# Optimization experiments

Hardware: AMD Instinct MI355X
Metric: run time of the kernel (lower is better)

## Reference

```python
import jax, jax.numpy as jnp
from jax import lax
import numpy as np

T, B, C, H = 2048, 512, 8, 20  # seq_len, batch, input channels, hidden size


def _lstm_layer(x_seq, W_ih, W_hh, b_ih, b_hh):
    """One unidirectional LSTM layer, PyTorch gate order (i, f, g, o).
    x_seq: [T, B, in], W_ih: [4H, in], W_hh: [4H, H]. Returns h sequence [T, B, H]."""
    Hh = W_hh.shape[1]
    # Precompute input contribution for all timesteps (batched GEMM, off the scan critical path)
    gx = jnp.einsum('tbc,gc->tbg', x_seq, W_ih) + b_ih + b_hh  # [T, B, 4H]

    def step(carry, g_t):
        h, c = carry
        g = g_t + h @ W_hh.T  # [B, 4H]
        i, f, gg, o = jnp.split(g, 4, axis=-1)
        i = jax.nn.sigmoid(i)
        f = jax.nn.sigmoid(f)
        gg = jnp.tanh(gg)
        o = jax.nn.sigmoid(o)
        c = f * c + i * gg
        h = o * jnp.tanh(c)
        return (h, c), h

    b = x_seq.shape[1]
    h0 = jnp.zeros((b, Hh), x_seq.dtype)
    c0 = jnp.zeros((b, Hh), x_seq.dtype)
    _, ys = lax.scan(step, (h0, c0), gx)
    return ys


def setup_inputs() -> dict:
    key = jax.random.key(0)
    ks = jax.random.split(key, 9)
    s = 1.0 / np.sqrt(H)  # PyTorch LSTM init scale
    return {
        'x': jax.random.normal(ks[0], (T, B, C), jnp.float32),
        'W_ih0': jax.random.uniform(ks[1], (4 * H, C), jnp.float32, -s, s),
        'W_hh0': jax.random.uniform(ks[2], (4 * H, H), jnp.float32, -s, s),
        'b_ih0': jax.random.uniform(ks[3], (4 * H,), jnp.float32, -s, s),
        'b_hh0': jax.random.uniform(ks[4], (4 * H,), jnp.float32, -s, s),
        'W_ih1': jax.random.uniform(ks[5], (4 * H, H), jnp.float32, -s, s),
        'W_hh1': jax.random.uniform(ks[6], (4 * H, H), jnp.float32, -s, s),
        'b_ih1': jax.random.uniform(ks[7], (4 * H,), jnp.float32, -s, s),
        'b_hh1': jax.random.uniform(ks[8], (4 * H,), jnp.float32, -s, s),
    }


def reference(x, W_ih0, W_hh0, b_ih0, b_hh0, W_ih1, W_hh1, b_ih1, b_hh1):
    # 2-layer LSTM with zero initial states; forward returns the full output sequence
    # (the fc head in the original module is unused in forward()).
    h1 = _lstm_layer(x, W_ih0, W_hh0, b_ih0, b_hh0)   # [T, B, H]
    out = _lstm_layer(h1, W_ih1, W_hh1, b_ih1, b_hh1)  # [T, B, H]
    return out
```

## Files before the change

kernel.cpp:

```cpp
#include <hip/hip_runtime.h>

namespace {

typedef float v2f __attribute__((ext_vector_type(2)));

constexpr int T_SEQ = 2048;
constexpr int B_SZ  = 512;
constexpr int C_IN  = 8;
constexpr int H_SZ  = 20;
constexpr int P_LEN = 16;
constexpr int N_PH  = T_SEQ / P_LEN;
constexpr int RING  = 2 * P_LEN;
constexpr float LOG2E = 1.44269504088896340736f;

__device__ __forceinline__ float rlane(float v, int lane) {
  return __int_as_float(__builtin_amdgcn_readlane(__float_as_int(v), lane));
}

template<int S>
__device__ __forceinline__ float quad_bcast(float v) {
  return __int_as_float(__builtin_amdgcn_update_dpp(
      __float_as_int(v), __float_as_int(v), S * 0x55, 0xF, 0xF, true));
}

__device__ __forceinline__ v2f fma2(v2f a, v2f b, v2f c) {
  return __builtin_elementwise_fma(a, b, c);
}
__device__ __forceinline__ v2f splat2(float s) { v2f r; r.x = s; r.y = s; return r; }
__device__ __forceinline__ v2f zero2() { v2f r; r.x = 0.f; r.y = 0.f; return r; }

__device__ __forceinline__ v2f act2(v2f a, float cm, float am, float ad) {
  float ex = __builtin_amdgcn_exp2f(a.x * cm);
  float ey = __builtin_amdgcn_exp2f(a.y * cm);
  float sx = __builtin_amdgcn_rcpf(1.0f + ex);
  float sy = __builtin_amdgcn_rcpf(1.0f + ey);
  v2f r; r.x = __fmaf_rn(sx, am, ad); r.y = __fmaf_rn(sy, am, ad);
  return r;
}

__device__ __forceinline__ float fast_tanh(float a) {
  float e = __builtin_amdgcn_exp2f(a * (-2.0f * LOG2E));
  float s = __builtin_amdgcn_rcpf(1.0f + e);
  return __fmaf_rn(s, 2.0f, -1.0f);
}

#define H_BCAST(ha, hb, k) (((k) < 16) ? rlane((ha), 4 * (k)) : rlane((hb), 4 * ((k) - 16)))

__global__ __attribute__((amdgpu_flat_work_group_size(128, 128),
                          amdgpu_waves_per_eu(1, 1)))
void lstm2_pk(const float* __restrict__ x,
              const float* __restrict__ Wih0, const float* __restrict__ Whh0,
              const float* __restrict__ bih0, const float* __restrict__ bhh0,
              const float* __restrict__ Wih1, const float* __restrict__ Whh1,
              const float* __restrict__ bih1, const float* __restrict__ bhh1,
              float* __restrict__ out)
{
  __shared__ __align__(16) float hbuf[RING][H_SZ];
  __shared__ __align__(16) float xbuf[2][P_LEN * C_IN];

  const int tid = threadIdx.x;
  const int wv  = tid >> 6;
  const int l   = tid & 63;
  const int b   = blockIdx.x;
  const int k1  = l >> 2;
  const int g   = l & 3;
  const int k2  = 16 + (k1 & 3);
  const int j1  = g * H_SZ + k1;
  const int j2  = g * H_SZ + k2;

  const bool  isg = (g == 2);
  const float cm  = isg ? (-2.0f * LOG2E) : (-LOG2E);
  const float am  = isg ?  2.0f : 1.0f;
  const float ad  = isg ? -1.0f : 0.0f;

  if (wv == 0) {
    v2f wx1[C_IN / 2], wx2[C_IN / 2];
    v2f wh[H_SZ];
#pragma unroll
    for (int t = 0; t < C_IN / 2; ++t) {
      wx1[t].x = Wih0[j1 * C_IN + 2 * t]; wx1[t].y = Wih0[j1 * C_IN + 2 * t + 1];
      wx2[t].x = Wih0[j2 * C_IN + 2 * t]; wx2[t].y = Wih0[j2 * C_IN + 2 * t + 1];
    }
#pragma unroll
    for (int k = 0; k < H_SZ; ++k) {
      wh[k].x = Whh0[j1 * H_SZ + k]; wh[k].y = Whh0[j2 * H_SZ + k];
    }
    v2f bias2; bias2.x = bih0[j1] + bhh0[j1]; bias2.y = bih0[j2] + bhh0[j2];

    float ha = 0.f, ca = 0.f, hb = 0.f, cb = 0.f;

    const float* xl = x + (size_t)(l >> 3) * (B_SZ * C_IN) + b * C_IN + (l & 7);
    const size_t halfph = (size_t)8 * B_SZ * C_IN;
    const size_t phstr  = (size_t)P_LEN * B_SZ * C_IN;

    {
      float v0 = xl[0], v1 = xl[halfph];
      xbuf[0][l] = v0; xbuf[0][64 + l] = v1;
    }
    float n0 = xl[phstr], n1 = xl[phstr + halfph];

    for (int p = 0; p <= N_PH; ++p) {
      if (p < N_PH) {
        const int buf = p & 1;
        float4 xc0 = ((const float4*)&xbuf[buf][0])[0];
        float4 xc1 = ((const float4*)&xbuf[buf][0])[1];
        for (int j = 0; j < P_LEN; ++j) {
          const int n = p * P_LEN + j;
          v2f xp[4];
          xp[0].x = xc0.x; xp[0].y = xc0.y; xp[1].x = xc0.z; xp[1].y = xc0.w;
          xp[2].x = xc1.x; xp[2].y = xc1.y; xp[3].x = xc1.z; xp[3].y = xc1.w;
          if (j + 1 < P_LEN) {
            xc0 = ((const float4*)&xbuf[buf][(j + 1) * C_IN])[0];
            xc1 = ((const float4*)&xbuf[buf][(j + 1) * C_IN])[1];
          }

          v2f A0 = bias2, A1 = zero2();
#pragma unroll
          for (int k = 0; k < H_SZ; k += 2) {
            float h0 = H_BCAST(ha, hb, k);
            float h1 = H_BCAST(ha, hb, k + 1);
            A0 = fma2(wh[k],     splat2(h0), A0);
            A1 = fma2(wh[k + 1], splat2(h1), A1);
          }
          v2f X1 = zero2(), X2 = zero2();
#pragma unroll
          for (int t = 0; t < C_IN / 2; ++t) {
            X1 = fma2(wx1[t], xp[t], X1);
            X2 = fma2(wx2[t], xp[t], X2);
          }
          v2f A = A0 + A1;
          A.x += X1.x + X1.y;
          A.y += X2.x + X2.y;

          v2f act = act2(A, cm, am, ad);
          float iv = quad_bcast<0>(act.x), fv = quad_bcast<1>(act.x);
          float gv = quad_bcast<2>(act.x), ov = quad_bcast<3>(act.x);
          ca = __fmaf_rn(fv, ca, iv * gv);
          ha = ov * fast_tanh(ca);
          iv = quad_bcast<0>(act.y); fv = quad_bcast<1>(act.y);
          gv = quad_bcast<2>(act.y); ov = quad_bcast<3>(act.y);
          cb = __fmaf_rn(fv, cb, iv * gv);
          hb = ov * fast_tanh(cb);

          const int slot = n & (RING - 1);
          if (g == 0) {
            hbuf[slot][k1] = ha;
            if (k1 < 4) hbuf[slot][16 + k1] = hb;
          }
        }
        if (p + 1 < N_PH) { xbuf[(p + 1) & 1][l] = n0; xbuf[(p + 1) & 1][64 + l] = n1; }
        if (p + 2 < N_PH) {
          n0 = xl[(size_t)(p + 2) * phstr];
          n1 = xl[(size_t)(p + 2) * phstr + halfph];
        }
      }
      __syncthreads();
    }
  } else {
    v2f wy1[H_SZ / 2], wy2[H_SZ / 2];
    v2f wq[H_SZ];
#pragma unroll
    for (int t = 0; t < H_SZ / 2; ++t) {
      wy1[t].x = Wih1[j1 * H_SZ + 2 * t]; wy1[t].y = Wih1[j1 * H_SZ + 2 * t + 1];
      wy2[t].x = Wih1[j2 * H_SZ + 2 * t]; wy2[t].y = Wih1[j2 * H_SZ + 2 * t + 1];
    }
#pragma unroll
    for (int k = 0; k < H_SZ; ++k) {
      wq[k].x = Whh1[j1 * H_SZ + k]; wq[k].y = Whh1[j2 * H_SZ + k];
    }
    v2f bias2; bias2.x = bih1[j1] + bhh1[j1]; bias2.y = bih1[j2] + bhh1[j2];

    float ha = 0.f, ca = 0.f, hb = 0.f, cb = 0.f;
    float* op = out + b * H_SZ;

    auto stepW1 = [&](int n, const float4 (&yq)[5]) {
      v2f yp[H_SZ / 2];
      yp[0].x = yq[0].x; yp[0].y = yq[0].y; yp[1].x = yq[0].z; yp[1].y = yq[0].w;
      yp[2].x = yq[1].x; yp[2].y = yq[1].y; yp[3].x = yq[1].z; yp[3].y = yq[1].w;
      yp[4].x = yq[2].x; yp[4].y = yq[2].y; yp[5].x = yq[2].z; yp[5].y = yq[2].w;
      yp[6].x = yq[3].x; yp[6].y = yq[3].y; yp[7].x = yq[3].z; yp[7].y = yq[3].w;
      yp[8].x = yq[4].x; yp[8].y = yq[4].y; yp[9].x = yq[4].z; yp[9].y = yq[4].w;

      v2f Y1a = zero2(), Y1b = zero2(), Y2a = zero2(), Y2b = zero2();
#pragma unroll
      for (int t = 0; t < H_SZ / 2; t += 2) {
        Y1a = fma2(wy1[t],     yp[t],     Y1a);
        Y2a = fma2(wy2[t],     yp[t],     Y2a);
        Y1b = fma2(wy1[t + 1], yp[t + 1], Y1b);
        Y2b = fma2(wy2[t + 1], yp[t + 1], Y2b);
      }
      v2f Q0 = bias2, Q1 = zero2();
#pragma unroll
      for (int k = 0; k < H_SZ; k += 2) {
        float q0 = H_BCAST(ha, hb, k);
        float q1 = H_BCAST(ha, hb, k + 1);
        Q0 = fma2(wq[k],     splat2(q0), Q0);
        Q1 = fma2(wq[k + 1], splat2(q1), Q1);
      }
      v2f A = Q0 + Q1;
      v2f Y1 = Y1a + Y1b, Y2 = Y2a + Y2b;
      A.x += Y1.x + Y1.y;
      A.y += Y2.x + Y2.y;

      v2f act = act2(A, cm, am, ad);
      float iv = quad_bcast<0>(act.x), fv = quad_bcast<1>(act.x);
      float gv = quad_bcast<2>(act.x), ov = quad_bcast<3>(act.x);
      ca = __fmaf_rn(fv, ca, iv * gv);
      ha = ov * fast_tanh(ca);
      iv = quad_bcast<0>(act.y); fv = quad_bcast<1>(act.y);
      gv = quad_bcast<2>(act.y); ov = quad_bcast<3>(act.y);
      cb = __fmaf_rn(fv, cb, iv * gv);
      hb = ov * fast_tanh(cb);

      if (g == 0) {
        op[k1] = ha;
        if (k1 < 4) op[16 + k1] = hb;
      }
      op += B_SZ * H_SZ;
    };

    for (int p = 0; p <= N_PH; ++p) {
      if (p >= 1) {
        const int base = (p - 1) * P_LEN;
        float4 yA[5], yB[5];
        {
          const float4* s = (const float4*)hbuf[base & (RING - 1)];
          yA[0] = s[0]; yA[1] = s[1]; yA[2] = s[2]; yA[3] = s[3]; yA[4] = s[4];
        }
        {
          const float4* s = (const float4*)hbuf[(base + 1) & (RING - 1)];
          yB[0] = s[0]; yB[1] = s[1]; yB[2] = s[2]; yB[3] = s[3]; yB[4] = s[4];
        }
        for (int jj = 0; jj < P_LEN; jj += 2) {
          stepW1(base + jj, yA);
          if (jj + 2 < P_LEN) {
            const float4* s = (const float4*)hbuf[(base + jj + 2) & (RING - 1)];
            yA[0] = s[0]; yA[1] = s[1]; yA[2] = s[2]; yA[3] = s[3]; yA[4] = s[4];
          }
          stepW1(base + jj + 1, yB);
          if (jj + 3 < P_LEN) {
            const float4* s = (const float4*)hbuf[(base + jj + 3) & (RING - 1)];
            yB[0] = s[0]; yB[1] = s[1]; yB[2] = s[2]; yB[3] = s[3]; yB[4] = s[4];
          }
        }
      }
      __syncthreads();
    }
  }
}

}

extern "C" void kernel_launch(void* const* d_in, const int* in_sizes, int n_in,
                              void* d_out, int out_size, void* d_ws, size_t ws_size,
                              hipStream_t stream) {
  const float* x    = (const float*)d_in[0];
  const float* Wih0 = (const float*)d_in[1];
  const float* Whh0 = (const float*)d_in[2];
  const float* bih0 = (const float*)d_in[3];
  const float* bhh0 = (const float*)d_in[4];
  const float* Wih1 = (const float*)d_in[5];
  const float* Whh1 = (const float*)d_in[6];
  const float* bih1 = (const float*)d_in[7];
  const float* bhh1 = (const float*)d_in[8];
  float* out = (float*)d_out;

  hipLaunchKernelGGL(lstm2_pk, dim3(B_SZ), dim3(128), 0, stream,
                     x, Wih0, Whh0, bih0, bhh0, Wih1, Whh1, bih1, bhh1, out);
}
```

Before: 704.4 us.

## Offload half of layer-1 input projection to layer-0 wave and rebalance recurrent FMAs

The layer-0 wave now computes the first 10 terms of layer 1's input projection (W_ih1 times h1) right after producing each h1, and passes the partial sums to the layer-1 wave through a new LDS ring buffer. This balances work between the two pipelined waves. Both waves now broadcast h once into a register array right after computing it, so the next step's recurrent dot product uses four independent accumulators instead of readlanes placed inside the FMA chain. The tanh*o product is also folded into a single fma. The layer-0 wave takes on extra FMAs, registers and LDS writes on its critical path.

```diff
diff --git a/kernel.cpp b/kernel.cpp
--- a/kernel.cpp
+++ b/kernel.cpp
@@ -12,6 +12,7 @@
 constexpr int N_PH  = T_SEQ / P_LEN;
 constexpr int RING  = 2 * P_LEN;
 constexpr float LOG2E = 1.44269504088896340736f;
+constexpr float M2 = -2.0f * LOG2E;
 
 __device__ __forceinline__ float rlane(float v, int lane) {
   return __int_as_float(__builtin_amdgcn_readlane(__float_as_int(v), lane));
@@ -37,14 +38,6 @@
   v2f r; r.x = __fmaf_rn(sx, am, ad); r.y = __fmaf_rn(sy, am, ad);
   return r;
 }
-
-__device__ __forceinline__ float fast_tanh(float a) {
-  float e = __builtin_amdgcn_exp2f(a * (-2.0f * LOG2E));
-  float s = __builtin_amdgcn_rcpf(1.0f + e);
-  return __fmaf_rn(s, 2.0f, -1.0f);
-}
-
-#define H_BCAST(ha, hb, k) (((k) < 16) ? rlane((ha), 4 * (k)) : rlane((hb), 4 * ((k) - 16)))
 
 __global__ __attribute__((amdgpu_flat_work_group_size(128, 128),
                           amdgpu_waves_per_eu(1, 1)))
@@ -56,6 +49,7 @@
               float* __restrict__ out)
 {
   __shared__ __align__(16) float hbuf[RING][H_SZ];
+  __shared__ __align__(16) v2f   pbuf[RING][64];
   __shared__ __align__(16) float xbuf[2][P_LEN * C_IN];
 
   const int tid = threadIdx.x;
@@ -76,6 +70,7 @@
   if (wv == 0) {
     v2f wx1[C_IN / 2], wx2[C_IN / 2];
     v2f wh[H_SZ];
+    v2f wp[10];
 #pragma unroll
     for (int t = 0; t < C_IN / 2; ++t) {
       wx1[t].x = Wih0[j1 * C_IN + 2 * t]; wx1[t].y = Wih0[j1 * C_IN + 2 * t + 1];
@@ -85,8 +80,15 @@
     for (int k = 0; k < H_SZ; ++k) {
       wh[k].x = Whh0[j1 * H_SZ + k]; wh[k].y = Whh0[j2 * H_SZ + k];
     }
+#pragma unroll
+    for (int k = 0; k < 10; ++k) {
+      wp[k].x = Wih1[j1 * H_SZ + k]; wp[k].y = Wih1[j2 * H_SZ + k];
+    }
     v2f bias2; bias2.x = bih0[j1] + bhh0[j1]; bias2.y = bih0[j2] + bhh0[j2];
 
+    float h_s[H_SZ];
+#pragma unroll
+    for (int k = 0; k < H_SZ; ++k) h_s[k] = 0.f;
     float ha = 0.f, ca = 0.f, hb = 0.f, cb = 0.f;
 
     const float* xl = x + (size_t)(l >> 3) * (B_SZ * C_IN) + b * C_IN + (l & 7);
@@ -114,39 +116,60 @@
             xc1 = ((const float4*)&xbuf[buf][(j + 1) * C_IN])[1];
           }
 
-          v2f A0 = bias2, A1 = zero2();
-#pragma unroll
-          for (int k = 0; k < H_SZ; k += 2) {
-            float h0 = H_BCAST(ha, hb, k);
-            float h1 = H_BCAST(ha, hb, k + 1);
-            A0 = fma2(wh[k],     splat2(h0), A0);
-            A1 = fma2(wh[k + 1], splat2(h1), A1);
-          }
           v2f X1 = zero2(), X2 = zero2();
 #pragma unroll
           for (int t = 0; t < C_IN / 2; ++t) {
             X1 = fma2(wx1[t], xp[t], X1);
             X2 = fma2(wx2[t], xp[t], X2);
           }
-          v2f A = A0 + A1;
-          A.x += X1.x + X1.y;
-          A.y += X2.x + X2.y;
+          v2f Xs; Xs.x = X1.x + X1.y; Xs.y = X2.x + X2.y;
+
+          v2f A0 = bias2, A1 = Xs, A2 = zero2(), A3 = zero2();
+#pragma unroll
+          for (int k = 0; k < H_SZ; k += 4) {
+            A0 = fma2(wh[k],     splat2(h_s[k]),     A0);
+            A1 = fma2(wh[k + 1], splat2(h_s[k + 1]), A1);
+            A2 = fma2(wh[k + 2], splat2(h_s[k + 2]), A2);
+            A3 = fma2(wh[k + 3], splat2(h_s[k + 3]), A3);
+          }
+          v2f A = (A0 + A1) + (A2 + A3);
 
           v2f act = act2(A, cm, am, ad);
           float iv = quad_bcast<0>(act.x), fv = quad_bcast<1>(act.x);
           float gv = quad_bcast<2>(act.x), ov = quad_bcast<3>(act.x);
           ca = __fmaf_rn(fv, ca, iv * gv);
-          ha = ov * fast_tanh(ca);
+          {
+            float e = __builtin_amdgcn_exp2f(ca * M2);
+            float r = __builtin_amdgcn_rcpf(1.0f + e);
+            ha = __fmaf_rn(r, ov + ov, -ov);
+          }
           iv = quad_bcast<0>(act.y); fv = quad_bcast<1>(act.y);
           gv = quad_bcast<2>(act.y); ov = quad_bcast<3>(act.y);
           cb = __fmaf_rn(fv, cb, iv * gv);
-          hb = ov * fast_tanh(cb);
+          {
+            float e = __builtin_amdgcn_exp2f(cb * M2);
+            float r = __builtin_amdgcn_rcpf(1.0f + e);
+            hb = __fmaf_rn(r, ov + ov, -ov);
+          }
 
           const int slot = n & (RING - 1);
           if (g == 0) {
             hbuf[slot][k1] = ha;
             if (k1 < 4) hbuf[slot][16 + k1] = hb;
           }
+
+#pragma unroll
+          for (int k = 0; k < 16; ++k) h_s[k] = rlane(ha, 4 * k);
+#pragma unroll
+          for (int k = 0; k < 4; ++k)  h_s[16 + k] = rlane(hb, 4 * k);
+
+          v2f P0 = zero2(), P1 = zero2();
+#pragma unroll
+          for (int k = 0; k < 10; k += 2) {
+            P0 = fma2(wp[k],     splat2(h_s[k]),     P0);
+            P1 = fma2(wp[k + 1], splat2(h_s[k + 1]), P1);
+          }
+          pbuf[slot][l] = P0 + P1;
         }
         if (p + 1 < N_PH) { xbuf[(p + 1) & 1][l] = n0; xbuf[(p + 1) & 1][64 + l] = n1; }
         if (p + 2 < N_PH) {
@@ -157,90 +180,111 @@
       __syncthreads();
     }
   } else {
-    v2f wy1[H_SZ / 2], wy2[H_SZ / 2];
+    v2f wy1[5], wy2[5];
+#pragma unroll
+    for (int t = 0; t < 5; ++t) {
+      wy1[t].x = Wih1[j1 * H_SZ + 10 + 2 * t]; wy1[t].y = Wih1[j1 * H_SZ + 11 + 2 * t];
+      wy2[t].x = Wih1[j2 * H_SZ + 10 + 2 * t]; wy2[t].y = Wih1[j2 * H_SZ + 11 + 2 * t];
+    }
     v2f wq[H_SZ];
-#pragma unroll
-    for (int t = 0; t < H_SZ / 2; ++t) {
-      wy1[t].x = Wih1[j1 * H_SZ + 2 * t]; wy1[t].y = Wih1[j1 * H_SZ + 2 * t + 1];
-      wy2[t].x = Wih1[j2 * H_SZ + 2 * t]; wy2[t].y = Wih1[j2 * H_SZ + 2 * t + 1];
-    }
 #pragma unroll
     for (int k = 0; k < H_SZ; ++k) {
       wq[k].x = Whh1[j1 * H_SZ + k]; wq[k].y = Whh1[j2 * H_SZ + k];
     }
     v2f bias2; bias2.x = bih1[j1] + bhh1[j1]; bias2.y = bih1[j2] + bhh1[j2];
 
+    float h_s[H_SZ];
+#pragma unroll
+    for (int k = 0; k < H_SZ; ++k) h_s[k] = 0.f;
     float ha = 0.f, ca = 0.f, hb = 0.f, cb = 0.f;
     float* op = out + b * H_SZ;
 
-    auto stepW1 = [&](int n, const float4 (&yq)[5]) {
-      v2f yp[H_SZ / 2];
-      yp[0].x = yq[0].x; yp[0].y = yq[0].y; yp[1].x = yq[0].z; yp[1].y = yq[0].w;
-      yp[2].x = yq[1].x; yp[2].y = yq[1].y; yp[3].x = yq[1].z; yp[3].y = yq[1].w;
-      yp[4].x = yq[2].x; yp[4].y = yq[2].y; yp[5].x = yq[2].z; yp[5].y = yq[2].w;
-      yp[6].x = yq[3].x; yp[6].y = yq[3].y; yp[7].x = yq[3].z; yp[7].y = yq[3].w;
-      yp[8].x = yq[4].x; yp[8].y = yq[4].y; yp[9].x = yq[4].z; yp[9].y = yq[4].w;
-
+    auto stepW1 = [&](const float4 (&yq)[3], v2f P) {
+      v2f yp[5];
+      yp[0].x = yq[0].z; yp[0].y = yq[0].w;
+      yp[1].x = yq[1].x; yp[1].y = yq[1].y;
+      yp[2].x = yq[1].z; yp[2].y = yq[1].w;
+      yp[3].x = yq[2].x; yp[3].y = yq[2].y;
+      yp[4].x = yq[2].z; yp[4].y = yq[2].w;
       v2f Y1a = zero2(), Y1b = zero2(), Y2a = zero2(), Y2b = zero2();
-#pragma unroll
-      for (int t = 0; t < H_SZ / 2; t += 2) {
-        Y1a = fma2(wy1[t],     yp[t],     Y1a);
-        Y2a = fma2(wy2[t],     yp[t],     Y2a);
-        Y1b = fma2(wy1[t + 1], yp[t + 1], Y1b);
-        Y2b = fma2(wy2[t + 1], yp[t + 1], Y2b);
-      }
-      v2f Q0 = bias2, Q1 = zero2();
-#pragma unroll
-      for (int k = 0; k < H_SZ; k += 2) {
-        float q0 = H_BCAST(ha, hb, k);
-        float q1 = H_BCAST(ha, hb, k + 1);
-        Q0 = fma2(wq[k],     splat2(q0), Q0);
-        Q1 = fma2(wq[k + 1], splat2(q1), Q1);
-      }
-      v2f A = Q0 + Q1;
+      Y1a = fma2(wy1[0], yp[0], Y1a); Y2a = fma2(wy2[0], yp[0], Y2a);
+      Y1b = fma2(wy1[1], yp[1], Y1b); Y2b = fma2(wy2[1], yp[1], Y2b);
+      Y1a = fma2(wy1[2], yp[2], Y1a); Y2a = fma2(wy2[2], yp[2], Y2a);
+      Y1b = fma2(wy1[3], yp[3], Y1b); Y2b = fma2(wy2[3], yp[3], Y2b);
+      Y1a = fma2(wy1[4], yp[4], Y1a); Y2a = fma2(wy2[4], yp[4], Y2a);
       v2f Y1 = Y1a + Y1b, Y2 = Y2a + Y2b;
-      A.x += Y1.x + Y1.y;
-      A.y += Y2.x + Y2.y;
+      v2f Ys; Ys.x = Y1.x + Y1.y; Ys.y = Y2.x + Y2.y;
+
+      v2f Q0 = bias2, Q1 = P, Q2 = Ys, Q3 = zero2();
+#pragma unroll
+      for (int k = 0; k < H_SZ; k += 4) {
+        Q0 = fma2(wq[k],     splat2(h_s[k]),     Q0);
+        Q1 = fma2(wq[k + 1], splat2(h_s[k + 1]), Q1);
+        Q2 = fma2(wq[k + 2], splat2(h_s[k + 2]), Q2);
+        Q3 = fma2(wq[k + 3], splat2(h_s[k + 3]), Q3);
+      }
+      v2f A = (Q0 + Q1) + (Q2 + Q3);
 
       v2f act = act2(A, cm, am, ad);
       float iv = quad_bcast<0>(act.x), fv = quad_bcast<1>(act.x);
       float gv = quad_bcast<2>(act.x), ov = quad_bcast<3>(act.x);
       ca = __fmaf_rn(fv, ca, iv * gv);
-      ha = ov * fast_tanh(ca);
+      {
+        float e = __builtin_amdgcn_exp2f(ca * M2);
+        float r = __builtin_amdgcn_rcpf(1.0f + e);
+        ha = __fmaf_rn(r, ov + ov, -ov);
+      }
       iv = quad_bcast<0>(act.y); fv = quad_bcast<1>(act.y);
       gv = quad_bcast<2>(act.y); ov = quad_bcast<3>(act.y);
       cb = __fmaf_rn(fv, cb, iv * gv);
-      hb = ov * fast_tanh(cb);
+      {
+        float e = __builtin_amdgcn_exp2f(cb * M2);
+        float r = __builtin_amdgcn_rcpf(1.0f + e);
+        hb = __fmaf_rn(r, ov + ov, -ov);
+      }
 
       if (g == 0) {
         op[k1] = ha;
         if (k1 < 4) op[16 + k1] = hb;
       }
       op += B_SZ * H_SZ;
+
+#pragma unroll
+      for (int k = 0; k < 16; ++k) h_s[k] = rlane(ha, 4 * k);
+#pragma unroll
+      for (int k = 0; k < 4; ++k)  h_s[16 + k] = rlane(hb, 4 * k);
     };
 
     for (int p = 0; p <= N_PH; ++p) {
       if (p >= 1) {
         const int base = (p - 1) * P_LEN;
-        float4 yA[5], yB[5];
+        float4 yA[3], yB[3]; v2f pA, pB;
         {
-          const float4* s = (const float4*)hbuf[base & (RING - 1)];
-          yA[0] = s[0]; yA[1] = s[1]; yA[2] = s[2]; yA[3] = s[3]; yA[4] = s[4];
+          const int s0 = base & (RING - 1);
+          const float4* s = (const float4*)hbuf[s0];
+          yA[0] = s[2]; yA[1] = s[3]; yA[2] = s[4];
+          pA = pbuf[s0][l];
         }
         {
-          const float4* s = (const float4*)hbuf[(base + 1) & (RING - 1)];
-          yB[0] = s[0]; yB[1] = s[1]; yB[2] = s[2]; yB[3] = s[3]; yB[4] = s[4];
+          const int s1 = (base + 1) & (RING - 1);
+          const float4* s = (const float4*)hbuf[s1];
+          yB[0] = s[2]; yB[1] = s[3]; yB[2] = s[4];
+          pB = pbuf[s1][l];
         }
         for (int jj = 0; jj < P_LEN; jj += 2) {
-          stepW1(base + jj, yA);
+          stepW1(yA, pA);
           if (jj + 2 < P_LEN) {
-            const float4* s = (const float4*)hbuf[(base + jj + 2) & (RING - 1)];
-            yA[0] = s[0]; yA[1] = s[1]; yA[2] = s[2]; yA[3] = s[3]; yA[4] = s[4];
-          }
-          stepW1(base + jj + 1, yB);
+            const int sn = (base + jj + 2) & (RING - 1);
+            const float4* s = (const float4*)hbuf[sn];
+            yA[0] = s[2]; yA[1] = s[3]; yA[2] = s[4];
+            pA = pbuf[sn][l];
+          }
+          stepW1(yB, pB);
           if (jj + 3 < P_LEN) {
-            const float4* s = (const float4*)hbuf[(base + jj + 3) & (RING - 1)];
-            yB[0] = s[0]; yB[1] = s[1]; yB[2] = s[2]; yB[3] = s[3]; yB[4] = s[4];
+            const int sn = (base + jj + 3) & (RING - 1);
+            const float4* s = (const float4*)hbuf[sn];
+            yB[0] = s[2]; yB[1] = s[3]; yB[2] = s[4];
+            pB = pbuf[sn][l];
           }
         }
       }
```

After: 731.6 us. 1.04x slower.

## Split LSTM into three-wave pipeline with dedicated input-projection wave

Applied to the files above, without the earlier changes.

Adds a third wavefront that computes the input projections (W_ih0·x and W_ih1·h1) for each phase ahead of time and stages them in shared-memory rings. The two recurrent waves then only do the hidden-state matvec and activations on the serial critical path. The aim is to take the input-GEMM work off the recurrence latency chain. The cost is an extra wave per block, more LDS, and a deeper three-stage barrier pipeline that adds two extra phases of sync.

```diff
diff --git a/kernel.cpp b/kernel.cpp
--- a/kernel.cpp
+++ b/kernel.cpp
@@ -46,9 +46,9 @@
 
 #define H_BCAST(ha, hb, k) (((k) < 16) ? rlane((ha), 4 * (k)) : rlane((hb), 4 * ((k) - 16)))
 
-__global__ __attribute__((amdgpu_flat_work_group_size(128, 128),
+__global__ __attribute__((amdgpu_flat_work_group_size(192, 192),
                           amdgpu_waves_per_eu(1, 1)))
-void lstm2_pk(const float* __restrict__ x,
+void lstm2_3w(const float* __restrict__ x,
               const float* __restrict__ Wih0, const float* __restrict__ Whh0,
               const float* __restrict__ bih0, const float* __restrict__ bhh0,
               const float* __restrict__ Wih1, const float* __restrict__ Whh1,
@@ -56,7 +56,9 @@
               float* __restrict__ out)
 {
   __shared__ __align__(16) float hbuf[RING][H_SZ];
-  __shared__ __align__(16) float xbuf[2][P_LEN * C_IN];
+  __shared__ __align__(16) v2f   ybuf[RING][64];
+  __shared__ __align__(16) v2f   xsbuf[RING][64];
+  __shared__ __align__(16) float xbuf[P_LEN * C_IN];
 
   const int tid = threadIdx.x;
   const int wv  = tid >> 6;
@@ -74,13 +76,7 @@
   const float ad  = isg ? -1.0f : 0.0f;
 
   if (wv == 0) {
-    v2f wx1[C_IN / 2], wx2[C_IN / 2];
     v2f wh[H_SZ];
-#pragma unroll
-    for (int t = 0; t < C_IN / 2; ++t) {
-      wx1[t].x = Wih0[j1 * C_IN + 2 * t]; wx1[t].y = Wih0[j1 * C_IN + 2 * t + 1];
-      wx2[t].x = Wih0[j2 * C_IN + 2 * t]; wx2[t].y = Wih0[j2 * C_IN + 2 * t + 1];
-    }
 #pragma unroll
     for (int k = 0; k < H_SZ; ++k) {
       wh[k].x = Whh0[j1 * H_SZ + k]; wh[k].y = Whh0[j2 * H_SZ + k];
@@ -89,32 +85,18 @@
 
     float ha = 0.f, ca = 0.f, hb = 0.f, cb = 0.f;
 
-    const float* xl = x + (size_t)(l >> 3) * (B_SZ * C_IN) + b * C_IN + (l & 7);
-    const size_t halfph = (size_t)8 * B_SZ * C_IN;
-    const size_t phstr  = (size_t)P_LEN * B_SZ * C_IN;
-
-    {
-      float v0 = xl[0], v1 = xl[halfph];
-      xbuf[0][l] = v0; xbuf[0][64 + l] = v1;
-    }
-    float n0 = xl[phstr], n1 = xl[phstr + halfph];
-
-    for (int p = 0; p <= N_PH; ++p) {
-      if (p < N_PH) {
-        const int buf = p & 1;
-        float4 xc0 = ((const float4*)&xbuf[buf][0])[0];
-        float4 xc1 = ((const float4*)&xbuf[buf][0])[1];
-        for (int j = 0; j < P_LEN; ++j) {
-          const int n = p * P_LEN + j;
-          v2f xp[4];
-          xp[0].x = xc0.x; xp[0].y = xc0.y; xp[1].x = xc0.z; xp[1].y = xc0.w;
-          xp[2].x = xc1.x; xp[2].y = xc1.y; xp[3].x = xc1.z; xp[3].y = xc1.w;
-          if (j + 1 < P_LEN) {
-            xc0 = ((const float4*)&xbuf[buf][(j + 1) * C_IN])[0];
-            xc1 = ((const float4*)&xbuf[buf][(j + 1) * C_IN])[1];
-          }
-
-          v2f A0 = bias2, A1 = zero2();
+    for (int s = 0; s <= N_PH + 2; ++s) {
+      if (s >= 1 && s <= N_PH) {
+        const int p0 = s - 1;
+        v2f XsCur = xsbuf[(p0 * P_LEN) & (RING - 1)][l];
+        for (int j = 0; j < P_LEN; ++j) {
+          const int n = p0 * P_LEN + j;
+          const int slot = n & (RING - 1);
+          v2f Xs = XsCur;
+          if (j + 1 < P_LEN)
+            XsCur = xsbuf[(n + 1) & (RING - 1)][l];
+
+          v2f A0 = bias2, A1 = Xs;
 #pragma unroll
           for (int k = 0; k < H_SZ; k += 2) {
             float h0 = H_BCAST(ha, hb, k);
@@ -122,15 +104,7 @@
             A0 = fma2(wh[k],     splat2(h0), A0);
             A1 = fma2(wh[k + 1], splat2(h1), A1);
           }
-          v2f X1 = zero2(), X2 = zero2();
-#pragma unroll
-          for (int t = 0; t < C_IN / 2; ++t) {
-            X1 = fma2(wx1[t], xp[t], X1);
-            X2 = fma2(wx2[t], xp[t], X2);
-          }
           v2f A = A0 + A1;
-          A.x += X1.x + X1.y;
-          A.y += X2.x + X2.y;
 
           v2f act = act2(A, cm, am, ad);
           float iv = quad_bcast<0>(act.x), fv = quad_bcast<1>(act.x);
@@ -142,28 +116,94 @@
           cb = __fmaf_rn(fv, cb, iv * gv);
           hb = ov * fast_tanh(cb);
 
-          const int slot = n & (RING - 1);
           if (g == 0) {
             hbuf[slot][k1] = ha;
             if (k1 < 4) hbuf[slot][16 + k1] = hb;
           }
         }
-        if (p + 1 < N_PH) { xbuf[(p + 1) & 1][l] = n0; xbuf[(p + 1) & 1][64 + l] = n1; }
-        if (p + 2 < N_PH) {
-          n0 = xl[(size_t)(p + 2) * phstr];
-          n1 = xl[(size_t)(p + 2) * phstr + halfph];
-        }
       }
       __syncthreads();
     }
-  } else {
+  } else if (wv == 1) {
+    v2f wx1[C_IN / 2], wx2[C_IN / 2];
     v2f wy1[H_SZ / 2], wy2[H_SZ / 2];
-    v2f wq[H_SZ];
+#pragma unroll
+    for (int t = 0; t < C_IN / 2; ++t) {
+      wx1[t].x = Wih0[j1 * C_IN + 2 * t]; wx1[t].y = Wih0[j1 * C_IN + 2 * t + 1];
+      wx2[t].x = Wih0[j2 * C_IN + 2 * t]; wx2[t].y = Wih0[j2 * C_IN + 2 * t + 1];
+    }
 #pragma unroll
     for (int t = 0; t < H_SZ / 2; ++t) {
       wy1[t].x = Wih1[j1 * H_SZ + 2 * t]; wy1[t].y = Wih1[j1 * H_SZ + 2 * t + 1];
       wy2[t].x = Wih1[j2 * H_SZ + 2 * t]; wy2[t].y = Wih1[j2 * H_SZ + 2 * t + 1];
     }
+
+    const float* xl = x + (size_t)(l >> 3) * (B_SZ * C_IN) + b * C_IN + (l & 7);
+    const size_t halfph = (size_t)8 * B_SZ * C_IN;
+    const size_t phstr  = (size_t)P_LEN * B_SZ * C_IN;
+
+    float cur0 = xl[0],     cur1 = xl[halfph];
+    float nx0  = xl[phstr], nx1  = xl[phstr + halfph];
+
+    for (int s = 0; s <= N_PH + 2; ++s) {
+      if (s <= N_PH - 1) {
+        xbuf[l] = cur0; xbuf[64 + l] = cur1;
+        asm volatile("s_waitcnt lgkmcnt(0)" ::: "memory");
+        float4 xc0 = ((const float4*)&xbuf[0])[0];
+        float4 xc1 = ((const float4*)&xbuf[0])[1];
+        for (int j = 0; j < P_LEN; ++j) {
+          v2f xp[4];
+          xp[0].x = xc0.x; xp[0].y = xc0.y; xp[1].x = xc0.z; xp[1].y = xc0.w;
+          xp[2].x = xc1.x; xp[2].y = xc1.y; xp[3].x = xc1.z; xp[3].y = xc1.w;
+          if (j + 1 < P_LEN) {
+            xc0 = ((const float4*)&xbuf[(j + 1) * C_IN])[0];
+            xc1 = ((const float4*)&xbuf[(j + 1) * C_IN])[1];
+          }
+          v2f X1 = zero2(), X2 = zero2();
+#pragma unroll
+          for (int t = 0; t < C_IN / 2; ++t) {
+            X1 = fma2(wx1[t], xp[t], X1);
+            X2 = fma2(wx2[t], xp[t], X2);
+          }
+          v2f Xs; Xs.x = X1.x + X1.y; Xs.y = X2.x + X2.y;
+          xsbuf[(s * P_LEN + j) & (RING - 1)][l] = Xs;
+        }
+        cur0 = nx0; cur1 = nx1;
+        if (s + 2 <= N_PH - 1) {
+          nx0 = xl[(size_t)(s + 2) * phstr];
+          nx1 = xl[(size_t)(s + 2) * phstr + halfph];
+        }
+      }
+      if (s >= 2 && s <= N_PH + 1) {
+        const int q = s - 2;
+        for (int j = 0; j < P_LEN; ++j) {
+          const int slot = (q * P_LEN + j) & (RING - 1);
+          const float4* sp = (const float4*)hbuf[slot];
+          float4 y0 = sp[0], y1 = sp[1], y2 = sp[2], y3 = sp[3], y4 = sp[4];
+          v2f yp[H_SZ / 2];
+          yp[0].x = y0.x; yp[0].y = y0.y; yp[1].x = y0.z; yp[1].y = y0.w;
+          yp[2].x = y1.x; yp[2].y = y1.y; yp[3].x = y1.z; yp[3].y = y1.w;
+          yp[4].x = y2.x; yp[4].y = y2.y; yp[5].x = y2.z; yp[5].y = y2.w;
+          yp[6].x = y3.x; yp[6].y = y3.y; yp[7].x = y3.z; yp[7].y = y3.w;
+          yp[8].x = y4.x; yp[8].y = y4.y; yp[9].x = y4.z; yp[9].y = y4.w;
+
+          v2f Y1a = zero2(), Y1b = zero2(), Y2a = zero2(), Y2b = zero2();
+#pragma unroll
+          for (int t = 0; t < H_SZ / 2; t += 2) {
+            Y1a = fma2(wy1[t],     yp[t],     Y1a);
+            Y2a = fma2(wy2[t],     yp[t],     Y2a);
+            Y1b = fma2(wy1[t + 1], yp[t + 1], Y1b);
+            Y2b = fma2(wy2[t + 1], yp[t + 1], Y2b);
+          }
+          v2f Y1 = Y1a + Y1b, Y2 = Y2a + Y2b;
+          v2f Ys; Ys.x = Y1.x + Y1.y; Ys.y = Y2.x + Y2.y;
+          ybuf[slot][l] = Ys;
+        }
+      }
+      __syncthreads();
+    }
+  } else {
+    v2f wq[H_SZ];
 #pragma unroll
     for (int k = 0; k < H_SZ; ++k) {
       wq[k].x = Whh1[j1 * H_SZ + k]; wq[k].y = Whh1[j2 * H_SZ + k];
@@ -173,75 +213,41 @@
     float ha = 0.f, ca = 0.f, hb = 0.f, cb = 0.f;
     float* op = out + b * H_SZ;
 
-    auto stepW1 = [&](int n, const float4 (&yq)[5]) {
-      v2f yp[H_SZ / 2];
-      yp[0].x = yq[0].x; yp[0].y = yq[0].y; yp[1].x = yq[0].z; yp[1].y = yq[0].w;
-      yp[2].x = yq[1].x; yp[2].y = yq[1].y; yp[3].x = yq[1].z; yp[3].y = yq[1].w;
-      yp[4].x = yq[2].x; yp[4].y = yq[2].y; yp[5].x = yq[2].z; yp[5].y = yq[2].w;
-      yp[6].x = yq[3].x; yp[6].y = yq[3].y; yp[7].x = yq[3].z; yp[7].y = yq[3].w;
-      yp[8].x = yq[4].x; yp[8].y = yq[4].y; yp[9].x = yq[4].z; yp[9].y = yq[4].w;
-
-      v2f Y1a = zero2(), Y1b = zero2(), Y2a = zero2(), Y2b = zero2();
-#pragma unroll
-      for (int t = 0; t < H_SZ / 2; t += 2) {
-        Y1a = fma2(wy1[t],     yp[t],     Y1a);
-        Y2a = fma2(wy2[t],     yp[t],     Y2a);
-        Y1b = fma2(wy1[t + 1], yp[t + 1], Y1b);
-        Y2b = fma2(wy2[t + 1], yp[t + 1], Y2b);
-      }
-      v2f Q0 = bias2, Q1 = zero2();
-#pragma unroll
-      for (int k = 0; k < H_SZ; k += 2) {
-        float q0 = H_BCAST(ha, hb, k);
-        float q1 = H_BCAST(ha, hb, k + 1);
-        Q0 = fma2(wq[k],     splat2(q0), Q0);
-        Q1 = fma2(wq[k + 1], splat2(q1), Q1);
-      }
-      v2f A = Q0 + Q1;
-      v2f Y1 = Y1a + Y1b, Y2 = Y2a + Y2b;
-      A.x += Y1.x + Y1.y;
-      A.y += Y2.x + Y2.y;
-
-      v2f act = act2(A, cm, am, ad);
-      float iv = quad_bcast<0>(act.x), fv = quad_bcast<1>(act.x);
-      float gv = quad_bcast<2>(act.x), ov = quad_bcast<3>(act.x);
-      ca = __fmaf_rn(fv, ca, iv * gv);
-      ha = ov * fast_tanh(ca);
-      iv = quad_bcast<0>(act.y); fv = quad_bcast<1>(act.y);
-      gv = quad_bcast<2>(act.y); ov = quad_bcast<3>(act.y);
-      cb = __fmaf_rn(fv, cb, iv * gv);
-      hb = ov * fast_tanh(cb);
-
-      if (g == 0) {
-        op[k1] = ha;
-        if (k1 < 4) op[16 + k1] = hb;
-      }
-      op += B_SZ * H_SZ;
-    };
-
-    for (int p = 0; p <= N_PH; ++p) {
-      if (p >= 1) {
-        const int base = (p - 1) * P_LEN;
-        float4 yA[5], yB[5];
-        {
-          const float4* s = (const float4*)hbuf[base & (RING - 1)];
-          yA[0] = s[0]; yA[1] = s[1]; yA[2] = s[2]; yA[3] = s[3]; yA[4] = s[4];
-        }
-        {
-          const float4* s = (const float4*)hbuf[(base + 1) & (RING - 1)];
-          yB[0] = s[0]; yB[1] = s[1]; yB[2] = s[2]; yB[3] = s[3]; yB[4] = s[4];
-        }
-        for (int jj = 0; jj < P_LEN; jj += 2) {
-          stepW1(base + jj, yA);
-          if (jj + 2 < P_LEN) {
-            const float4* s = (const float4*)hbuf[(base + jj + 2) & (RING - 1)];
-            yA[0] = s[0]; yA[1] = s[1]; yA[2] = s[2]; yA[3] = s[3]; yA[4] = s[4];
-          }
-          stepW1(base + jj + 1, yB);
-          if (jj + 3 < P_LEN) {
-            const float4* s = (const float4*)hbuf[(base + jj + 3) & (RING - 1)];
-            yB[0] = s[0]; yB[1] = s[1]; yB[2] = s[2]; yB[3] = s[3]; yB[4] = s[4];
-          }
+    for (int s = 0; s <= N_PH + 2; ++s) {
+      if (s >= 3) {
+        const int r = s - 3;
+        v2f YsCur = ybuf[(r * P_LEN) & (RING - 1)][l];
+        for (int j = 0; j < P_LEN; ++j) {
+          const int n = r * P_LEN + j;
+          v2f Ys = YsCur;
+          if (j + 1 < P_LEN)
+            YsCur = ybuf[(n + 1) & (RING - 1)][l];
+
+          v2f Q0 = bias2, Q1 = Ys;
+#pragma unroll
+          for (int k = 0; k < H_SZ; k += 2) {
+            float q0 = H_BCAST(ha, hb, k);
+            float q1 = H_BCAST(ha, hb, k + 1);
+            Q0 = fma2(wq[k],     splat2(q0), Q0);
+            Q1 = fma2(wq[k + 1], splat2(q1), Q1);
+          }
+          v2f A = Q0 + Q1;
+
+          v2f act = act2(A, cm, am, ad);
+          float iv = quad_bcast<0>(act.x), fv = quad_bcast<1>(act.x);
+          float gv = quad_bcast<2>(act.x), ov = quad_bcast<3>(act.x);
+          ca = __fmaf_rn(fv, ca, iv * gv);
+          ha = ov * fast_tanh(ca);
+          iv = quad_bcast<0>(act.y); fv = quad_bcast<1>(act.y);
+          gv = quad_bcast<2>(act.y); ov = quad_bcast<3>(act.y);
+          cb = __fmaf_rn(fv, cb, iv * gv);
+          hb = ov * fast_tanh(cb);
+
+          if (g == 0) {
+            op[k1] = ha;
+            if (k1 < 4) op[16 + k1] = hb;
+          }
+          op += B_SZ * H_SZ;
         }
       }
       __syncthreads();
@@ -265,6 +271,6 @@
   const float* bhh1 = (const float*)d_in[8];
   float* out = (float*)d_out;
 
-  hipLaunchKernelGGL(lstm2_pk, dim3(B_SZ), dim3(128), 0, stream,
+  hipLaunchKernelGGL(lstm2_3w, dim3(B_SZ), dim3(192), 0, stream,
                      x, Wih0, Whh0, bih0, bhh0, Wih1, Whh1, bih1, bhh1, out);
 }
```

After: 1.091 ms. 1.55x slower.

## Pack four batch elements per 512-thread workgroup with per-pair shared buffers

Applied to the files above, without the earlier changes.

Each workgroup now handles four batch elements: eight waves form four producer/consumer pairs, each with its own slice of the h ring buffer and x buffer. The grid shrinks to B/4 blocks and waves_per_eu goes from 1 to 2. This changes how the 512 independent recurrences map onto CUs and SIMDs, aiming for better latency hiding and less per-block overhead. The cost is that __syncthreads now couples all four pairs, so each pair waits on the slowest of the group, and register budget per wave may tighten under the 2-waves-per-EU bound.

```diff
diff --git a/kernel.cpp b/kernel.cpp
--- a/kernel.cpp
+++ b/kernel.cpp
@@ -11,6 +11,7 @@
 constexpr int P_LEN = 16;
 constexpr int N_PH  = T_SEQ / P_LEN;
 constexpr int RING  = 2 * P_LEN;
+constexpr int QB    = 4;
 constexpr float LOG2E = 1.44269504088896340736f;
 
 __device__ __forceinline__ float rlane(float v, int lane) {
@@ -46,34 +47,36 @@
 
 #define H_BCAST(ha, hb, k) (((k) < 16) ? rlane((ha), 4 * (k)) : rlane((hb), 4 * ((k) - 16)))
 
-__global__ __attribute__((amdgpu_flat_work_group_size(128, 128),
-                          amdgpu_waves_per_eu(1, 1)))
-void lstm2_pk(const float* __restrict__ x,
-              const float* __restrict__ Wih0, const float* __restrict__ Whh0,
-              const float* __restrict__ bih0, const float* __restrict__ bhh0,
-              const float* __restrict__ Wih1, const float* __restrict__ Whh1,
-              const float* __restrict__ bih1, const float* __restrict__ bhh1,
-              float* __restrict__ out)
+__global__ __attribute__((amdgpu_flat_work_group_size(512, 512),
+                          amdgpu_waves_per_eu(2, 2)))
+void lstm2_pair(const float* __restrict__ x,
+                const float* __restrict__ Wih0, const float* __restrict__ Whh0,
+                const float* __restrict__ bih0, const float* __restrict__ bhh0,
+                const float* __restrict__ Wih1, const float* __restrict__ Whh1,
+                const float* __restrict__ bih1, const float* __restrict__ bhh1,
+                float* __restrict__ out)
 {
-  __shared__ __align__(16) float hbuf[RING][H_SZ];
-  __shared__ __align__(16) float xbuf[2][P_LEN * C_IN];
-
-  const int tid = threadIdx.x;
-  const int wv  = tid >> 6;
-  const int l   = tid & 63;
-  const int b   = blockIdx.x;
-  const int k1  = l >> 2;
-  const int g   = l & 3;
-  const int k2  = 16 + (k1 & 3);
-  const int j1  = g * H_SZ + k1;
-  const int j2  = g * H_SZ + k2;
+  __shared__ __align__(16) float hbuf[QB][RING][H_SZ];
+  __shared__ __align__(16) float xbuf[QB][2][P_LEN * C_IN];
+
+  const int tid  = threadIdx.x;
+  const int wv   = tid >> 6;
+  const int q    = wv >> 1;
+  const int role = wv & 1;
+  const int l    = tid & 63;
+  const int b    = blockIdx.x * QB + q;
+  const int k1   = l >> 2;
+  const int g    = l & 3;
+  const int k2   = 16 + (k1 & 3);
+  const int j1   = g * H_SZ + k1;
+  const int j2   = g * H_SZ + k2;
 
   const bool  isg = (g == 2);
   const float cm  = isg ? (-2.0f * LOG2E) : (-LOG2E);
   const float am  = isg ?  2.0f : 1.0f;
   const float ad  = isg ? -1.0f : 0.0f;
 
-  if (wv == 0) {
+  if (role == 0) {
     v2f wx1[C_IN / 2], wx2[C_IN / 2];
     v2f wh[H_SZ];
 #pragma unroll
@@ -95,23 +98,23 @@
 
     {
       float v0 = xl[0], v1 = xl[halfph];
-      xbuf[0][l] = v0; xbuf[0][64 + l] = v1;
+      xbuf[q][0][l] = v0; xbuf[q][0][64 + l] = v1;
     }
     float n0 = xl[phstr], n1 = xl[phstr + halfph];
 
     for (int p = 0; p <= N_PH; ++p) {
       if (p < N_PH) {
         const int buf = p & 1;
-        float4 xc0 = ((const float4*)&xbuf[buf][0])[0];
-        float4 xc1 = ((const float4*)&xbuf[buf][0])[1];
+        float4 xc0 = ((const float4*)&xbuf[q][buf][0])[0];
+        float4 xc1 = ((const float4*)&xbuf[q][buf][0])[1];
         for (int j = 0; j < P_LEN; ++j) {
           const int n = p * P_LEN + j;
           v2f xp[4];
           xp[0].x = xc0.x; xp[0].y = xc0.y; xp[1].x = xc0.z; xp[1].y = xc0.w;
           xp[2].x = xc1.x; xp[2].y = xc1.y; xp[3].x = xc1.z; xp[3].y = xc1.w;
           if (j + 1 < P_LEN) {
-            xc0 = ((const float4*)&xbuf[buf][(j + 1) * C_IN])[0];
-            xc1 = ((const float4*)&xbuf[buf][(j + 1) * C_IN])[1];
+            xc0 = ((const float4*)&xbuf[q][buf][(j + 1) * C_IN])[0];
+            xc1 = ((const float4*)&xbuf[q][buf][(j + 1) * C_IN])[1];
           }
 
           v2f A0 = bias2, A1 = zero2();
@@ -144,11 +147,11 @@
 
           const int slot = n & (RING - 1);
           if (g == 0) {
-            hbuf[slot][k1] = ha;
-            if (k1 < 4) hbuf[slot][16 + k1] = hb;
-          }
-        }
-        if (p + 1 < N_PH) { xbuf[(p + 1) & 1][l] = n0; xbuf[(p + 1) & 1][64 + l] = n1; }
+            hbuf[q][slot][k1] = ha;
+            if (k1 < 4) hbuf[q][slot][16 + k1] = hb;
+          }
+        }
+        if (p + 1 < N_PH) { xbuf[q][(p + 1) & 1][l] = n0; xbuf[q][(p + 1) & 1][64 + l] = n1; }
         if (p + 2 < N_PH) {
           n0 = xl[(size_t)(p + 2) * phstr];
           n1 = xl[(size_t)(p + 2) * phstr + halfph];
@@ -224,22 +227,22 @@
         const int base = (p - 1) * P_LEN;
         float4 yA[5], yB[5];
         {
-          const float4* s = (const float4*)hbuf[base & (RING - 1)];
+          const float4* s = (const float4*)hbuf[q][base & (RING - 1)];
           yA[0] = s[0]; yA[1] = s[1]; yA[2] = s[2]; yA[3] = s[3]; yA[4] = s[4];
         }
         {
-          const float4* s = (const float4*)hbuf[(base + 1) & (RING - 1)];
+          const float4* s = (const float4*)hbuf[q][(base + 1) & (RING - 1)];
           yB[0] = s[0]; yB[1] = s[1]; yB[2] = s[2]; yB[3] = s[3]; yB[4] = s[4];
         }
         for (int jj = 0; jj < P_LEN; jj += 2) {
           stepW1(base + jj, yA);
           if (jj + 2 < P_LEN) {
-            const float4* s = (const float4*)hbuf[(base + jj + 2) & (RING - 1)];
+            const float4* s = (const float4*)hbuf[q][(base + jj + 2) & (RING - 1)];
             yA[0] = s[0]; yA[1] = s[1]; yA[2] = s[2]; yA[3] = s[3]; yA[4] = s[4];
           }
           stepW1(base + jj + 1, yB);
           if (jj + 3 < P_LEN) {
-            const float4* s = (const float4*)hbuf[(base + jj + 3) & (RING - 1)];
+            const float4* s = (const float4*)hbuf[q][(base + jj + 3) & (RING - 1)];
             yB[0] = s[0]; yB[1] = s[1]; yB[2] = s[2]; yB[3] = s[3]; yB[4] = s[4];
           }
         }
@@ -265,6 +268,6 @@
   const float* bhh1 = (const float*)d_in[8];
   float* out = (float*)d_out;
 
-  hipLaunchKernelGGL(lstm2_pk, dim3(B_SZ), dim3(128), 0, stream,
+  hipLaunchKernelGGL(lstm2_pair, dim3(B_SZ / QB), dim3(512), 0, stream,
                      x, Wih0, Whh0, bih0, bhh0, Wih1, Whh1, bih1, bhh1, out);
 }
```

Result: slower. 1.031 ms (+46.3%).
